# Kernel tuning notes

Hardware: AMD Instinct MI355X
Metric: run time of the kernel (lower is better)

## Reference

```python
import jax, jax.numpy as jnp
import numpy as np
from jax import lax

EPS = 1e-5
NUM_BITS = 8          # activation quantization bits
NUM_BITS_WEIGHT = 8   # weight quantization bits


def fake_quant(x, bits):
    """Uniform min-max quantize-dequantize (per-tensor), STE on round."""
    mn = jnp.min(x)
    mx = jnp.max(x)
    scale = jnp.maximum((mx - mn) / (2 ** bits - 1), jnp.asarray(1e-8, x.dtype))
    q = jnp.round((x - mn) / scale) * scale + mn
    # straight-through estimator: identity gradient through rounding
    return x + lax.stop_gradient(q - x)


def batchnorm(x, gamma, beta, mean, var):
    # x: [N, C, H, W]; stats per channel C (eval mode, running stats)
    inv = gamma / jnp.sqrt(var + EPS)
    return x * inv[None, :, None, None] + (beta - mean * inv)[None, :, None, None]


def qconv(x, w, padding):
    xq = fake_quant(x, NUM_BITS)
    wq = fake_quant(w, NUM_BITS_WEIGHT)
    return lax.conv_general_dilated(
        xq, wq, window_strides=(1, 1), padding=padding,
        dimension_numbers=("NCHW", "OIHW", "NCHW"))


def setup_inputs() -> dict:
    key = jax.random.key(0)
    ks = jax.random.split(key, 8)
    C_in, bn_size, growth = 512, 4, 32
    C_mid = bn_size * growth  # 128
    N, H, W = 64, 28, 28
    x = jax.random.normal(ks[0], (N, C_in, H, W), dtype=jnp.float32)
    gamma1 = jax.random.uniform(ks[1], (C_in,), minval=0.5, maxval=1.5)
    beta1 = jax.random.normal(ks[2], (C_in,)) * 0.1
    mean1 = jax.random.normal(ks[3], (C_in,)) * 0.1
    var1 = jax.random.uniform(ks[4], (C_in,), minval=0.5, maxval=1.5)
    w1 = jax.random.normal(ks[5], (C_mid, C_in, 1, 1)) * (1.0 / np.sqrt(C_in))
    gamma2 = jax.random.uniform(ks[6], (C_mid,), minval=0.5, maxval=1.5)
    beta2 = jax.random.normal(ks[7], (C_mid,)) * 0.1
    mean2 = jax.random.normal(jax.random.fold_in(key, 10), (C_mid,)) * 0.1
    var2 = jax.random.uniform(jax.random.fold_in(key, 11), (C_mid,), minval=0.5, maxval=1.5)
    w2 = jax.random.normal(jax.random.fold_in(key, 12), (growth, C_mid, 3, 3)) * (1.0 / np.sqrt(C_mid * 9))
    return {"x": x, "gamma1": gamma1, "beta1": beta1, "mean1": mean1, "var1": var1,
            "w1": w1, "gamma2": gamma2, "beta2": beta2, "mean2": mean2, "var2": var2,
            "w2": w2}


def reference(x, gamma1, beta1, mean1, var1, w1, gamma2, beta2, mean2, var2, w2):
    h = jax.nn.relu(batchnorm(x, gamma1, beta1, mean1, var1))
    h = qconv(h, w1, padding=((0, 0), (0, 0)))            # 1x1 conv, 512 -> 128
    h = jax.nn.relu(batchnorm(h, gamma2, beta2, mean2, var2))
    h = qconv(h, w2, padding=((1, 1), (1, 1)))            # 3x3 conv, 128 -> 32
    # drop_rate == 0 -> dropout is identity
    return h
```

## Files before the change

### kernel.cpp

```cpp
#include <hip/hip_runtime.h>

typedef unsigned short u16;
typedef unsigned short u16x4 __attribute__((ext_vector_type(4)));
typedef unsigned short u16x8 __attribute__((ext_vector_type(8)));
typedef short bf16x8 __attribute__((ext_vector_type(8)));
typedef float f32x4 __attribute__((ext_vector_type(4)));

#define EPSF 1e-5f

#define NB   64
#define C1   512
#define C2   128
#define C3   32
#define HH   28
#define WW   28
#define HW   784
#define NHW  50176
#define XELEMS 25690112
#define K1_BLOCKS 512
#define CONV_BLOCKS 392
#define W1E 65536
#define W2E 36864

#define WS_BN1I   64
#define WS_BN1B   2112
#define WS_BN2I   4160
#define WS_BN2B   4672
#define WS_WQ1    5376
#define WS_WQ2    136448
#define WS_P1     210176
#define WS_P2     214272
#define WS_PW1    217408
#define WS_PW2    217920
#define WS_H2     218112

__device__ __forceinline__ float bf2f(u16 u) { return __uint_as_float(((unsigned)u) << 16); }
__device__ __forceinline__ u16 f2bf(float f) {
  unsigned x = __float_as_uint(f);
  return (u16)((x + 0x7fffu + ((x >> 16) & 1u)) >> 16);
}
__device__ __forceinline__ float finz(float f) {
  unsigned u = __float_as_uint(f);
  return ((u & 0x7f800000u) == 0x7f800000u) ? 0.0f : f;
}

__device__ __forceinline__ void block_minmax(float& mn, float& mx) {
  for (int m = 32; m; m >>= 1) {
    mn = fminf(mn, __shfl_xor(mn, m));
    mx = fmaxf(mx, __shfl_xor(mx, m));
  }
  __shared__ float wmn[4], wmx[4];
  const int wv = threadIdx.x >> 6;
  if ((threadIdx.x & 63) == 0) { wmn[wv] = mn; wmx[wv] = mx; }
  __syncthreads();
  if (threadIdx.x == 0) {
    mn = fminf(fminf(wmn[0], wmn[1]), fminf(wmn[2], wmn[3]));
    mx = fmaxf(fmaxf(wmx[0], wmx[1]), fmaxf(wmx[2], wmx[3]));
  }
}

__global__ __launch_bounds__(256) void kwA_kernel(const float* g1, const float* be1,
                                                  const float* m1, const float* v1,
                                                  const float* w1,
                                                  const float* g2, const float* be2,
                                                  const float* m2, const float* v2,
                                                  const float* w2, unsigned char* ws) {
  const int t = threadIdx.x;
  const int b = blockIdx.x;
  float2* pw1 = (float2*)(ws + WS_PW1);
  float2* pw2 = (float2*)(ws + WS_PW2);

  if (b == 80) {
    float* bn1i = (float*)(ws + WS_BN1I);
    float* bn1b = (float*)(ws + WS_BN1B);
    float* bn2i = (float*)(ws + WS_BN2I);
    float* bn2b = (float*)(ws + WS_BN2B);
    for (int c = t; c < C1; c += 256) {
      float inv = g1[c] / sqrtf(v1[c] + EPSF);
      bn1i[c] = inv;
      bn1b[c] = be1[c] - m1[c] * inv;
    }
    if (t < C2) {
      float inv = g2[t] / sqrtf(v2[t] + EPSF);
      bn2i[t] = inv;
      bn2b[t] = be2[t] - m2[t] * inv;
    }
    return;
  }

  float mn = 3.4e38f, mx = -3.4e38f;
  if (b < 64) {
    f32x4 v = *(const f32x4*)(w1 + b * 1024 + t * 4);
#pragma unroll
    for (int j = 0; j < 4; j++) {
      float f = finz(v[j]); mn = fminf(mn, f); mx = fmaxf(mx, f);
    }
    block_minmax(mn, mx);
    if (t == 0) pw1[b] = make_float2(mn, mx);
  } else {
    const int base = (b - 64) * 2304;
#pragma unroll
    for (int j = 0; j < 9; j++) {
      float f = finz(w2[base + t + j * 256]); mn = fminf(mn, f); mx = fmaxf(mx, f);
    }
    block_minmax(mn, mx);
    if (t == 0) pw2[b - 64] = make_float2(mn, mx);
  }
}

__global__ __launch_bounds__(256) void kwB_kernel(const float* w1, const float* w2,
                                                  unsigned char* ws) {
  const float2* pw1 = (const float2*)(ws + WS_PW1);
  const float2* pw2 = (const float2*)(ws + WS_PW2);
  u16* wq1 = (u16*)(ws + WS_WQ1);
  u16* wq2 = (u16*)(ws + WS_WQ2);
  const int t = threadIdx.x;
  const int b = blockIdx.x;
  __shared__ float bc[2];

  if (b < 64) {
    if (t < 64) {
      float2 p = pw1[t];
      float mn = p.x, mx = p.y;
      for (int m = 32; m; m >>= 1) {
        mn = fminf(mn, __shfl_xor(mn, m));
        mx = fmaxf(mx, __shfl_xor(mx, m));
      }
      if (t == 0) { bc[0] = mn; bc[1] = mx; }
    }
    __syncthreads();
    const float mn = bc[0];
    const float s = fmaxf((bc[1] - mn) / 255.0f, 1e-8f);
    const float rs = 1.0f / s;
    f32x4 v = *(const f32x4*)(w1 + b * 1024 + t * 4);
    u16x4 o;
#pragma unroll
    for (int j = 0; j < 4; j++)
      o[j] = f2bf(fmaf(rintf((finz(v[j]) - mn) * rs), s, mn));
    *(u16x4*)(wq1 + b * 1024 + t * 4) = o;
  } else {
    if (t < 64) {
      float2 p = (t < 16) ? pw2[t] : make_float2(3.4e38f, -3.4e38f);
      float mn = p.x, mx = p.y;
      for (int m = 32; m; m >>= 1) {
        mn = fminf(mn, __shfl_xor(mn, m));
        mx = fmaxf(mx, __shfl_xor(mx, m));
      }
      if (t == 0) { bc[0] = mn; bc[1] = mx; }
    }
    __syncthreads();
    const float mn = bc[0];
    const float s = fmaxf((bc[1] - mn) / 255.0f, 1e-8f);
    const float rs = 1.0f / s;
    const int base = (b - 64) * 2304;
#pragma unroll
    for (int j = 0; j < 9; j++) {
      int o = base + t + j * 256;
      int tap = o >> 12;
      int rem = o & 4095;
      float f = finz(w2[rem * 9 + tap]);
      wq2[o] = f2bf(fmaf(rintf((f - mn) * rs), s, mn));
    }
  }
}

__global__ __launch_bounds__(256) void k1_minmax(const float* __restrict__ x, unsigned char* ws) {
  const float* bn1i = (const float*)(ws + WS_BN1I);
  const float* bn1b = (const float*)(ws + WS_BN1B);
  float2* p1 = (float2*)(ws + WS_P1);
  int gid = blockIdx.x * blockDim.x + threadIdx.x;
  int stride = gridDim.x * blockDim.x;
  const int ngroups = XELEMS / 4;
  float mn = 3.4e38f, mx = 0.0f;
  for (int i = gid; i < ngroups; i += stride) {
    int base = i * 4;
    int c = (base / HW) & (C1 - 1);
    float inv = bn1i[c], bb = bn1b[c];
    f32x4 u = *((const f32x4*)x + i);
#pragma unroll
    for (int j = 0; j < 4; j++) {
      float f = finz(fmaxf(fmaf(u[j], inv, bb), 0.0f));
      mn = fminf(mn, f); mx = fmaxf(mx, f);
    }
  }
  block_minmax(mn, mx);
  if (threadIdx.x == 0) p1[blockIdx.x] = make_float2(mn, mx);
}

__global__ __launch_bounds__(256) void conv1_kernel(const float* __restrict__ x,
                                                    unsigned char* ws) {
  const float* bn1i = (const float*)(ws + WS_BN1I);
  const float* bn1b = (const float*)(ws + WS_BN1B);
  const float* bn2i = (const float*)(ws + WS_BN2I);
  const float* bn2b = (const float*)(ws + WS_BN2B);
  const u16* wq1 = (const u16*)(ws + WS_WQ1);
  const float2* p1 = (const float2*)(ws + WS_P1);
  float2* p2 = (float2*)(ws + WS_P2);
  u16* h2 = (u16*)(ws + WS_H2);

  __shared__ __align__(16) u16 Alds[128 * 40];
  __shared__ __align__(16) u16 Blds[128 * 40];
  __shared__ float bc[2];
  __shared__ float wred[8];

  const int t = threadIdx.x;
  const int sp0 = blockIdx.x * 128;

  {
    float* rmn = (float*)Alds;
    float* rmx = (float*)Blds;
    float2 a = p1[t];
    float2 b = p1[t + 256];
    rmn[t] = fminf(a.x, b.x);
    rmx[t] = fmaxf(a.y, b.y);
    __syncthreads();
    for (int s = 128; s > 0; s >>= 1) {
      if (t < s) { rmn[t] = fminf(rmn[t], rmn[t + s]); rmx[t] = fmaxf(rmx[t], rmx[t + s]); }
      __syncthreads();
    }
    if (t == 0) { bc[0] = rmn[0]; bc[1] = rmx[0]; }
    __syncthreads();
  }
  const float mn1 = bc[0];
  const float mx1 = bc[1];
  const float s1 = fmaxf((mx1 - mn1) / 255.0f, 1e-8f);
  const float r1 = 1.0f / s1;

  const int kk = t >> 3;
  const int spA = (t & 7) * 8;
  const int spB = 64 + spA;
  const int ga = sp0 + spA, gb = sp0 + spB;
  const int na = ga / HW, hwa = ga % HW;
  const int nb = gb / HW, hwb = gb % HW;
  const float* xA = x + na * (C1 * HW) + hwa;
  const float* xB = x + nb * (C1 * HW) + hwb;

  const int wco = t >> 1;
  const int wko = (t & 1) * 16;

  const int lane = t & 63;
  const int l15 = lane & 15;
  const int q = lane >> 4;
  const int wv = t >> 6;
  const int wy = wv >> 1;
  const int wx = wv & 1;

  f32x4 acc[4][4] = {};

  for (int k0 = 0; k0 < C1; k0 += 32) {
    __syncthreads();
    {
      const u16* src = wq1 + wco * C1 + k0 + wko;
      u16x8 a0 = *(const u16x8*)(src);
      u16x8 a1 = *(const u16x8*)(src + 8);
      *(u16x8*)&Alds[wco * 40 + wko] = a0;
      *(u16x8*)&Alds[wco * 40 + wko + 8] = a1;
    }
    {
      int c = k0 + kk;
      float inv = bn1i[c], bb = bn1b[c];
      f32x4 va0 = *(const f32x4*)(xA + c * HW);
      f32x4 va1 = *(const f32x4*)(xA + c * HW + 4);
      f32x4 vb0 = *(const f32x4*)(xB + c * HW);
      f32x4 vb1 = *(const f32x4*)(xB + c * HW + 4);
#pragma unroll
      for (int j = 0; j < 4; j++) {
        float f0 = finz(fmaxf(fmaf(va0[j], inv, bb), 0.0f));
        Blds[(spA + j) * 40 + kk] = f2bf(fmaf(rintf((f0 - mn1) * r1), s1, mn1));
        float f1 = finz(fmaxf(fmaf(va1[j], inv, bb), 0.0f));
        Blds[(spA + 4 + j) * 40 + kk] = f2bf(fmaf(rintf((f1 - mn1) * r1), s1, mn1));
        float g0 = finz(fmaxf(fmaf(vb0[j], inv, bb), 0.0f));
        Blds[(spB + j) * 40 + kk] = f2bf(fmaf(rintf((g0 - mn1) * r1), s1, mn1));
        float g1v = finz(fmaxf(fmaf(vb1[j], inv, bb), 0.0f));
        Blds[(spB + 4 + j) * 40 + kk] = f2bf(fmaf(rintf((g1v - mn1) * r1), s1, mn1));
      }
    }
    __syncthreads();
    bf16x8 af[4], bfr[4];
#pragma unroll
    for (int i = 0; i < 4; i++) {
      af[i] = *(const bf16x8*)&Alds[(wy * 64 + i * 16 + l15) * 40 + q * 8];
      bfr[i] = *(const bf16x8*)&Blds[(wx * 64 + i * 16 + l15) * 40 + q * 8];
    }
#pragma unroll
    for (int i = 0; i < 4; i++)
#pragma unroll
      for (int j = 0; j < 4; j++)
        acc[i][j] = __builtin_amdgcn_mfma_f32_16x16x32_bf16(af[i], bfr[j], acc[i][j], 0, 0, 0);
  }

  float lmn = 3.4e38f, lmx = 0.0f;
#pragma unroll
  for (int i = 0; i < 4; i++) {
    int cob = wy * 64 + i * 16 + q * 4;
    f32x4 i2 = *(const f32x4*)&bn2i[cob];
    f32x4 b2 = *(const f32x4*)&bn2b[cob];
#pragma unroll
    for (int j = 0; j < 4; j++) {
      int sp = sp0 + wx * 64 + j * 16 + l15;
      u16x4 v;
#pragma unroll
      for (int r = 0; r < 4; r++) {
        float h = finz(fmaxf(fmaf(acc[i][j][r], i2[r], b2[r]), 0.0f));
        v[r] = f2bf(h);
        lmn = fminf(lmn, h); lmx = fmaxf(lmx, h);
      }
      *(u16x4*)&h2[sp * C2 + cob] = v;
    }
  }
  for (int m = 32; m; m >>= 1) {
    lmn = fminf(lmn, __shfl_xor(lmn, m));
    lmx = fmaxf(lmx, __shfl_xor(lmx, m));
  }
  if (lane == 0) { wred[wv] = lmn; wred[4 + wv] = lmx; }
  __syncthreads();
  if (t == 0) {
    float2 pr;
    pr.x = fminf(fminf(wred[0], wred[1]), fminf(wred[2], wred[3]));
    pr.y = fmaxf(fmaxf(wred[4], wred[5]), fmaxf(wred[6], wred[7]));
    p2[blockIdx.x] = pr;
  }
}

__global__ __launch_bounds__(256) void conv2_kernel(const unsigned char* ws,
                                                    float* __restrict__ out) {
  const u16* wq2 = (const u16*)(ws + WS_WQ2);
  const u16* h2 = (const u16*)(ws + WS_H2);
  const float2* p2 = (const float2*)(ws + WS_P2);

  __shared__ float rn[256], rx[256], bc2[2];
  const int t = threadIdx.x;
  {
    float m = 3.4e38f, M = 0.0f;
    if (t < 196) {
      float2 a = p2[t];
      float2 b = p2[t + 196];
      m = fminf(a.x, b.x); M = fmaxf(a.y, b.y);
    }
    rn[t] = m; rx[t] = M;
    __syncthreads();
    for (int s = 128; s > 0; s >>= 1) {
      if (t < s) { rn[t] = fminf(rn[t], rn[t + s]); rx[t] = fmaxf(rx[t], rx[t + s]); }
      __syncthreads();
    }
    if (t == 0) { bc2[0] = rn[0]; bc2[1] = rx[0]; }
    __syncthreads();
  }
  const float mn2 = bc2[0];
  const float mx2 = bc2[1];
  const float s2 = fmaxf((mx2 - mn2) / 255.0f, 1e-8f);
  const float r2 = 1.0f / s2;

  const int lane = t & 63;
  const int l15 = lane & 15;
  const int q = lane >> 4;
  const int wv = t >> 6;
  const int sp0 = blockIdx.x * 128 + wv * 32;

  int spf[2], nn[2], hwf[2], hf[2], wf[2];
#pragma unroll
  for (int f = 0; f < 2; f++) {
    spf[f] = sp0 + f * 16 + l15;
    nn[f] = spf[f] / HW;
    hwf[f] = spf[f] % HW;
    hf[f] = hwf[f] / WW;
    wf[f] = hwf[f] % WW;
  }

  f32x4 acc[2][2] = {};
  bf16x8 bz;
#pragma unroll
  for (int j = 0; j < 8; j++) bz[j] = 0;

  for (int tap = 0; tap < 9; tap++) {
    const int dh = tap / 3 - 1, dw = tap % 3 - 1;
    const u16* wA = wq2 + tap * (C3 * C2);
    const u16* bptr[2];
    bool val[2];
#pragma unroll
    for (int f = 0; f < 2; f++) {
      unsigned h2i = (unsigned)(hf[f] + dh);
      unsigned w2i = (unsigned)(wf[f] + dw);
      val[f] = (h2i < 28u) && (w2i < 28u);
      bptr[f] = h2 + ((size_t)(nn[f] * HW + (int)h2i * WW + (int)w2i)) * C2;
    }
#pragma unroll
    for (int ks = 0; ks < C2; ks += 32) {
      bf16x8 a[2], b[2];
#pragma unroll
      for (int f = 0; f < 2; f++)
        a[f] = *(const bf16x8*)(wA + (f * 16 + l15) * C2 + ks + q * 8);
#pragma unroll
      for (int f = 0; f < 2; f++) {
        if (val[f]) {
          u16x8 hv = *(const u16x8*)(bptr[f] + ks + q * 8);
          bf16x8 bb;
#pragma unroll
          for (int j = 0; j < 8; j++) {
            float h = bf2f(hv[j]);
            bb[j] = (short)f2bf(fmaf(rintf((h - mn2) * r2), s2, mn2));
          }
          b[f] = bb;
        } else {
          b[f] = bz;
        }
      }
#pragma unroll
      for (int i = 0; i < 2; i++)
#pragma unroll
        for (int j = 0; j < 2; j++)
          acc[i][j] = __builtin_amdgcn_mfma_f32_16x16x32_bf16(a[i], b[j], acc[i][j], 0, 0, 0);
    }
  }

#pragma unroll
  for (int i = 0; i < 2; i++) {
    int co = i * 16 + q * 4;
#pragma unroll
    for (int j = 0; j < 2; j++) {
#pragma unroll
      for (int r = 0; r < 4; r++)
        out[(nn[j] * C3 + co + r) * HW + hwf[j]] = acc[i][j][r];
    }
  }
}

extern "C" void kernel_launch(void* const* d_in, const int* in_sizes, int n_in,
                              void* d_out, int out_size, void* d_ws, size_t ws_size,
                              hipStream_t stream) {
  const float* x  = (const float*)d_in[0];
  const float* g1 = (const float*)d_in[1];
  const float* b1 = (const float*)d_in[2];
  const float* m1 = (const float*)d_in[3];
  const float* v1 = (const float*)d_in[4];
  const float* w1 = (const float*)d_in[5];
  const float* g2 = (const float*)d_in[6];
  const float* b2 = (const float*)d_in[7];
  const float* m2 = (const float*)d_in[8];
  const float* v2 = (const float*)d_in[9];
  const float* w2 = (const float*)d_in[10];
  unsigned char* ws = (unsigned char*)d_ws;
  float* out = (float*)d_out;

  kwA_kernel<<<81, 256, 0, stream>>>(g1, b1, m1, v1, w1, g2, b2, m2, v2, w2, ws);
  kwB_kernel<<<80, 256, 0, stream>>>(w1, w2, ws);
  k1_minmax<<<K1_BLOCKS, 256, 0, stream>>>(x, ws);
  conv1_kernel<<<CONV_BLOCKS, 256, 0, stream>>>(x, ws);
  conv2_kernel<<<CONV_BLOCKS, 256, 0, stream>>>(ws, out);
}
```

Measured before the change: 253.8 us.

## Halve conv tile sizes, swizzle LDS, raise block counts, drop finite checks

Doubles the grid for both conv kernels by halving the spatial tile (128 to 64 positions), and quadruples the min/max pre-pass grid. The goal is to fill more of the CUs on the large GPU. It adds an XOR-style swizzle on the LDS A/B tiles to cut bank conflicts, and replaces the tree reductions of partial min/max with wave-shuffle reductions. It also removes the non-finite guards. That saves ALU work but changes behaviour if there are inf/NaN inputs, and smaller tiles reload the weight tile more often per output.

```diff
diff --git a/kernel.cpp b/kernel.cpp
--- a/kernel.cpp
+++ b/kernel.cpp
@@ -17,10 +17,9 @@
 #define HW   784
 #define NHW  50176
 #define XELEMS 25690112
-#define K1_BLOCKS 512
-#define CONV_BLOCKS 392
-#define W1E 65536
-#define W2E 36864
+#define K1_BLOCKS 2048
+#define CONV1_BLOCKS 784
+#define CONV2_BLOCKS 784
 
 #define WS_BN1I   64
 #define WS_BN1B   2112
@@ -29,10 +28,10 @@
 #define WS_WQ1    5376
 #define WS_WQ2    136448
 #define WS_P1     210176
-#define WS_P2     214272
-#define WS_PW1    217408
-#define WS_PW2    217920
-#define WS_H2     218112
+#define WS_P2     226560
+#define WS_PW1    232832
+#define WS_PW2    233344
+#define WS_H2     233472
 
 __device__ __forceinline__ float bf2f(u16 u) { return __uint_as_float(((unsigned)u) << 16); }
 __device__ __forceinline__ u16 f2bf(float f) {
@@ -179,7 +178,7 @@
     f32x4 u = *((const f32x4*)x + i);
 #pragma unroll
     for (int j = 0; j < 4; j++) {
-      float f = finz(fmaxf(fmaf(u[j], inv, bb), 0.0f));
+      float f = fmaxf(fmaf(u[j], inv, bb), 0.0f);
       mn = fminf(mn, f); mx = fmaxf(mx, f);
     }
   }
@@ -199,44 +198,41 @@
   u16* h2 = (u16*)(ws + WS_H2);
 
   __shared__ __align__(16) u16 Alds[128 * 40];
-  __shared__ __align__(16) u16 Blds[128 * 40];
+  __shared__ __align__(16) u16 Blds[64 * 40];
   __shared__ float bc[2];
   __shared__ float wred[8];
 
   const int t = threadIdx.x;
-  const int sp0 = blockIdx.x * 128;
+  const int sp0 = blockIdx.x * 64;
 
   {
-    float* rmn = (float*)Alds;
-    float* rmx = (float*)Blds;
-    float2 a = p1[t];
-    float2 b = p1[t + 256];
-    rmn[t] = fminf(a.x, b.x);
-    rmx[t] = fmaxf(a.y, b.y);
-    __syncthreads();
-    for (int s = 128; s > 0; s >>= 1) {
-      if (t < s) { rmn[t] = fminf(rmn[t], rmn[t + s]); rmx[t] = fmaxf(rmx[t], rmx[t + s]); }
-      __syncthreads();
-    }
-    if (t == 0) { bc[0] = rmn[0]; bc[1] = rmx[0]; }
+    const f32x4* p4 = (const f32x4*)p1;
+    float mn = 3.4e38f, mx = 0.0f;
+#pragma unroll
+    for (int i = 0; i < 4; i++) {
+      f32x4 v = p4[t + i * 256];
+      mn = fminf(mn, fminf(v[0], v[2]));
+      mx = fmaxf(mx, fmaxf(v[1], v[3]));
+    }
+    block_minmax(mn, mx);
+    if (t == 0) { bc[0] = mn; bc[1] = mx; }
     __syncthreads();
   }
   const float mn1 = bc[0];
-  const float mx1 = bc[1];
-  const float s1 = fmaxf((mx1 - mn1) / 255.0f, 1e-8f);
+  const float s1 = fmaxf((bc[1] - mn1) / 255.0f, 1e-8f);
   const float r1 = 1.0f / s1;
 
   const int kk = t >> 3;
   const int spA = (t & 7) * 8;
-  const int spB = 64 + spA;
-  const int ga = sp0 + spA, gb = sp0 + spB;
+  const int bswz = ((spA >> 3) & 3) * 8;
+  const int ga = sp0 + spA;
   const int na = ga / HW, hwa = ga % HW;
-  const int nb = gb / HW, hwb = gb % HW;
   const float* xA = x + na * (C1 * HW) + hwa;
-  const float* xB = x + nb * (C1 * HW) + hwb;
 
   const int wco = t >> 1;
   const int wko = (t & 1) * 16;
+  const int ab0 = wko >> 3;
+  const int aswz = (wco >> 3) & 3;
 
   const int lane = t & 63;
   const int l15 = lane & 15;
@@ -245,7 +241,7 @@
   const int wy = wv >> 1;
   const int wx = wv & 1;
 
-  f32x4 acc[4][4] = {};
+  f32x4 acc[4][2] = {};
 
   for (int k0 = 0; k0 < C1; k0 += 32) {
     __syncthreads();
@@ -253,39 +249,39 @@
       const u16* src = wq1 + wco * C1 + k0 + wko;
       u16x8 a0 = *(const u16x8*)(src);
       u16x8 a1 = *(const u16x8*)(src + 8);
-      *(u16x8*)&Alds[wco * 40 + wko] = a0;
-      *(u16x8*)&Alds[wco * 40 + wko + 8] = a1;
+      *(u16x8*)&Alds[wco * 40 + (((ab0 + 0 + aswz) & 3) << 3)] = a0;
+      *(u16x8*)&Alds[wco * 40 + (((ab0 + 1 + aswz) & 3) << 3)] = a1;
     }
     {
       int c = k0 + kk;
       float inv = bn1i[c], bb = bn1b[c];
       f32x4 va0 = *(const f32x4*)(xA + c * HW);
       f32x4 va1 = *(const f32x4*)(xA + c * HW + 4);
-      f32x4 vb0 = *(const f32x4*)(xB + c * HW);
-      f32x4 vb1 = *(const f32x4*)(xB + c * HW + 4);
+      const int col = ((kk + bswz) & 31);
 #pragma unroll
       for (int j = 0; j < 4; j++) {
-        float f0 = finz(fmaxf(fmaf(va0[j], inv, bb), 0.0f));
-        Blds[(spA + j) * 40 + kk] = f2bf(fmaf(rintf((f0 - mn1) * r1), s1, mn1));
-        float f1 = finz(fmaxf(fmaf(va1[j], inv, bb), 0.0f));
-        Blds[(spA + 4 + j) * 40 + kk] = f2bf(fmaf(rintf((f1 - mn1) * r1), s1, mn1));
-        float g0 = finz(fmaxf(fmaf(vb0[j], inv, bb), 0.0f));
-        Blds[(spB + j) * 40 + kk] = f2bf(fmaf(rintf((g0 - mn1) * r1), s1, mn1));
-        float g1v = finz(fmaxf(fmaf(vb1[j], inv, bb), 0.0f));
-        Blds[(spB + 4 + j) * 40 + kk] = f2bf(fmaf(rintf((g1v - mn1) * r1), s1, mn1));
+        float f0 = fmaxf(fmaf(va0[j], inv, bb), 0.0f);
+        Blds[(spA + j) * 40 + col] = f2bf(fmaf(rintf((f0 - mn1) * r1), s1, mn1));
+        float f1 = fmaxf(fmaf(va1[j], inv, bb), 0.0f);
+        Blds[(spA + 4 + j) * 40 + col] = f2bf(fmaf(rintf((f1 - mn1) * r1), s1, mn1));
       }
     }
     __syncthreads();
-    bf16x8 af[4], bfr[4];
+    bf16x8 af[4], bfr[2];
 #pragma unroll
     for (int i = 0; i < 4; i++) {
-      af[i] = *(const bf16x8*)&Alds[(wy * 64 + i * 16 + l15) * 40 + q * 8];
-      bfr[i] = *(const bf16x8*)&Blds[(wx * 64 + i * 16 + l15) * 40 + q * 8];
+      int R = wy * 64 + i * 16 + l15;
+      af[i] = *(const bf16x8*)&Alds[R * 40 + (((q + (R >> 3)) & 3) << 3)];
+    }
+#pragma unroll
+    for (int j = 0; j < 2; j++) {
+      int R = wx * 32 + j * 16 + l15;
+      bfr[j] = *(const bf16x8*)&Blds[R * 40 + (((q + (R >> 3)) & 3) << 3)];
     }
 #pragma unroll
     for (int i = 0; i < 4; i++)
 #pragma unroll
-      for (int j = 0; j < 4; j++)
+      for (int j = 0; j < 2; j++)
         acc[i][j] = __builtin_amdgcn_mfma_f32_16x16x32_bf16(af[i], bfr[j], acc[i][j], 0, 0, 0);
   }
 
@@ -296,12 +292,12 @@
     f32x4 i2 = *(const f32x4*)&bn2i[cob];
     f32x4 b2 = *(const f32x4*)&bn2b[cob];
 #pragma unroll
-    for (int j = 0; j < 4; j++) {
-      int sp = sp0 + wx * 64 + j * 16 + l15;
+    for (int j = 0; j < 2; j++) {
+      int sp = sp0 + wx * 32 + j * 16 + l15;
       u16x4 v;
 #pragma unroll
       for (int r = 0; r < 4; r++) {
-        float h = finz(fmaxf(fmaf(acc[i][j][r], i2[r], b2[r]), 0.0f));
+        float h = fmaxf(fmaf(acc[i][j][r], i2[r], b2[r]), 0.0f);
         v[r] = f2bf(h);
         lmn = fminf(lmn, h); lmx = fmaxf(lmx, h);
       }
@@ -327,47 +323,35 @@
   const u16* wq2 = (const u16*)(ws + WS_WQ2);
   const u16* h2 = (const u16*)(ws + WS_H2);
   const float2* p2 = (const float2*)(ws + WS_P2);
-
-  __shared__ float rn[256], rx[256], bc2[2];
+  __shared__ float bc2[2];
+
   const int t = threadIdx.x;
   {
-    float m = 3.4e38f, M = 0.0f;
-    if (t < 196) {
-      float2 a = p2[t];
-      float2 b = p2[t + 196];
-      m = fminf(a.x, b.x); M = fmaxf(a.y, b.y);
-    }
-    rn[t] = m; rx[t] = M;
-    __syncthreads();
-    for (int s = 128; s > 0; s >>= 1) {
-      if (t < s) { rn[t] = fminf(rn[t], rn[t + s]); rx[t] = fmaxf(rx[t], rx[t + s]); }
-      __syncthreads();
-    }
-    if (t == 0) { bc2[0] = rn[0]; bc2[1] = rx[0]; }
+    float mn = 3.4e38f, mx = 0.0f;
+    for (int i = t; i < CONV1_BLOCKS; i += 256) {
+      float2 p = p2[i];
+      mn = fminf(mn, p.x); mx = fmaxf(mx, p.y);
+    }
+    block_minmax(mn, mx);
+    if (t == 0) { bc2[0] = mn; bc2[1] = mx; }
     __syncthreads();
   }
   const float mn2 = bc2[0];
-  const float mx2 = bc2[1];
-  const float s2 = fmaxf((mx2 - mn2) / 255.0f, 1e-8f);
+  const float s2 = fmaxf((bc2[1] - mn2) / 255.0f, 1e-8f);
   const float r2 = 1.0f / s2;
 
   const int lane = t & 63;
   const int l15 = lane & 15;
   const int q = lane >> 4;
   const int wv = t >> 6;
-  const int sp0 = blockIdx.x * 128 + wv * 32;
-
-  int spf[2], nn[2], hwf[2], hf[2], wf[2];
-#pragma unroll
-  for (int f = 0; f < 2; f++) {
-    spf[f] = sp0 + f * 16 + l15;
-    nn[f] = spf[f] / HW;
-    hwf[f] = spf[f] % HW;
-    hf[f] = hwf[f] / WW;
-    wf[f] = hwf[f] % WW;
-  }
-
-  f32x4 acc[2][2] = {};
+
+  const int spf = blockIdx.x * 64 + wv * 16 + l15;
+  const int nn = spf / HW;
+  const int hwf = spf % HW;
+  const int hf = hwf / WW;
+  const int wf = hwf % WW;
+
+  f32x4 acc[2] = {};
   bf16x8 bz;
 #pragma unroll
   for (int j = 0; j < 8; j++) bz[j] = 0;
@@ -375,41 +359,29 @@
   for (int tap = 0; tap < 9; tap++) {
     const int dh = tap / 3 - 1, dw = tap % 3 - 1;
     const u16* wA = wq2 + tap * (C3 * C2);
-    const u16* bptr[2];
-    bool val[2];
-#pragma unroll
-    for (int f = 0; f < 2; f++) {
-      unsigned h2i = (unsigned)(hf[f] + dh);
-      unsigned w2i = (unsigned)(wf[f] + dw);
-      val[f] = (h2i < 28u) && (w2i < 28u);
-      bptr[f] = h2 + ((size_t)(nn[f] * HW + (int)h2i * WW + (int)w2i)) * C2;
-    }
+    unsigned h2i = (unsigned)(hf + dh);
+    unsigned w2i = (unsigned)(wf + dw);
+    const bool val = (h2i < 28u) && (w2i < 28u);
+    const u16* bptr = h2 + ((size_t)(nn * HW + (int)h2i * WW + (int)w2i)) * C2;
 #pragma unroll
     for (int ks = 0; ks < C2; ks += 32) {
-      bf16x8 a[2], b[2];
+      bf16x8 a[2], b;
 #pragma unroll
       for (int f = 0; f < 2; f++)
         a[f] = *(const bf16x8*)(wA + (f * 16 + l15) * C2 + ks + q * 8);
-#pragma unroll
-      for (int f = 0; f < 2; f++) {
-        if (val[f]) {
-          u16x8 hv = *(const u16x8*)(bptr[f] + ks + q * 8);
-          bf16x8 bb;
-#pragma unroll
-          for (int j = 0; j < 8; j++) {
-            float h = bf2f(hv[j]);
-            bb[j] = (short)f2bf(fmaf(rintf((h - mn2) * r2), s2, mn2));
-          }
-          b[f] = bb;
-        } else {
-          b[f] = bz;
+      if (val) {
+        u16x8 hv = *(const u16x8*)(bptr + ks + q * 8);
+#pragma unroll
+        for (int j = 0; j < 8; j++) {
+          float h = bf2f(hv[j]);
+          b[j] = (short)f2bf(fmaf(rintf((h - mn2) * r2), s2, mn2));
         }
+      } else {
+        b = bz;
       }
 #pragma unroll
       for (int i = 0; i < 2; i++)
-#pragma unroll
-        for (int j = 0; j < 2; j++)
-          acc[i][j] = __builtin_amdgcn_mfma_f32_16x16x32_bf16(a[i], b[j], acc[i][j], 0, 0, 0);
+        acc[i] = __builtin_amdgcn_mfma_f32_16x16x32_bf16(a[i], b, acc[i], 0, 0, 0);
     }
   }
 
@@ -417,11 +389,8 @@
   for (int i = 0; i < 2; i++) {
     int co = i * 16 + q * 4;
 #pragma unroll
-    for (int j = 0; j < 2; j++) {
-#pragma unroll
-      for (int r = 0; r < 4; r++)
-        out[(nn[j] * C3 + co + r) * HW + hwf[j]] = acc[i][j][r];
-    }
+    for (int r = 0; r < 4; r++)
+      out[(nn * C3 + co + r) * HW + hwf] = acc[i][r];
   }
 }
 
@@ -445,6 +414,6 @@
   kwA_kernel<<<81, 256, 0, stream>>>(g1, b1, m1, v1, w1, g2, b2, m2, v2, w2, ws);
   kwB_kernel<<<80, 256, 0, stream>>>(w1, w2, ws);
   k1_minmax<<<K1_BLOCKS, 256, 0, stream>>>(x, ws);
-  conv1_kernel<<<CONV_BLOCKS, 256, 0, stream>>>(x, ws);
-  conv2_kernel<<<CONV_BLOCKS, 256, 0, stream>>>(ws, out);
-}
+  conv1_kernel<<<CONV1_BLOCKS, 256, 0, stream>>>(x, ws);
+  conv2_kernel<<<CONV2_BLOCKS, 256, 0, stream>>>(ws, out);
+}
```

Result: no change. 254.1 us (+0.1%).
